# Performance work log

Hardware: AMD Instinct MI355X
Metric: run time of the kernel (lower is better)

Reference implementation:

```python
import jax, jax.numpy as jnp
import numpy as np

B, N, D, H = 4096, 64, 32, 64

def setup_inputs() -> dict:
    key = jax.random.key(0)
    ks = jax.random.split(key, 10)
    s = lambda fan_in: 1.0 / np.sqrt(fan_in)
    return {
        "joint_features": jax.random.normal(ks[0], (B, N, D), jnp.float32),
        "Wm1": jax.random.uniform(ks[1], (2 * D, H), jnp.float32, -s(2 * D), s(2 * D)),
        "bm1": jax.random.uniform(ks[2], (H,), jnp.float32, -s(2 * D), s(2 * D)),
        "Wm2": jax.random.uniform(ks[3], (H, D), jnp.float32, -s(H), s(H)),
        "bm2": jax.random.uniform(ks[4], (D,), jnp.float32, -s(H), s(H)),
        "Wu1": jax.random.uniform(ks[5], (2 * D, H), jnp.float32, -s(2 * D), s(2 * D)),
        "bu1": jax.random.uniform(ks[6], (H,), jnp.float32, -s(2 * D), s(2 * D)),
        "Wu2": jax.random.uniform(ks[7], (H, D), jnp.float32, -s(H), s(H)),
        "bu2": jax.random.uniform(ks[8], (D,), jnp.float32, -s(H), s(H)),
        "residual_weight": jnp.float32(0.5),
        "num_joints": N,
    }

def reference(joint_features, Wm1, bm1, Wm2, bm2, Wu1, bu1, Wu2, bu2, residual_weight, num_joints):
    n = num_joints
    # chain topology: directed edges (i->i+1) and (i+1->i); dst receives message
    dst = jnp.concatenate([jnp.arange(n - 1), jnp.arange(1, n)])  # [E]
    src = jnp.concatenate([jnp.arange(1, n), jnp.arange(n - 1)])  # [E]
    # edge gather + concat: [B, E, 2D]
    edge_in = jnp.concatenate([joint_features[:, dst], joint_features[:, src]], axis=-1)
    # message MLP (ReLU after both layers, per original Sequential)
    msg = jax.nn.relu(jax.nn.relu(edge_in @ Wm1 + bm1) @ Wm2 + bm2)  # [B, E, D]
    # scatter-add messages to destination nodes
    messages = jnp.zeros_like(joint_features).at[:, dst].add(msg)  # [B, N, D]
    # per-node update MLP on concat(feature, message)
    upd_in = jnp.concatenate([joint_features, messages], axis=-1)  # [B, N, 2D]
    updated = jax.nn.relu(upd_in @ Wu1 + bu1) @ Wu2 + bu2  # [B, N, D]
    return residual_weight * updated + (1.0 - residual_weight) * joint_features
```

## Files before the change

kernel.cpp:

```cpp
#include <hip/hip_runtime.h>
#include <hip/hip_bf16.h>


typedef __bf16 bf16x8 __attribute__((ext_vector_type(8)));
typedef float  f32x4  __attribute__((ext_vector_type(4)));
typedef unsigned short u16;

#define NBATCH 8
#define ITERS (NBATCH / 2)
#define HS 72
#define MS 40

#define FB2_OFF 0
#define FB3_OFF (FB2_OFF + 4 * 512)
#define FB4_OFF (FB3_OFF + 8 * 512)
#define SH_OFF   0
#define SM_OFF   (SH_OFF + 256 * HS)
#define BIAS_OFF (SM_OFF + 128 * MS)
#define SMEM_U16 (BIAS_OFF + 384)

__device__ __forceinline__ u16 f2b(float f) { return __builtin_bit_cast(u16, (__bf16)f); }
__device__ __forceinline__ f32x4 MFMA(bf16x8 a, bf16x8 b, f32x4 c) {
    return __builtin_amdgcn_mfma_f32_16x16x32_bf16(a, b, c, 0, 0, 0);
}
__device__ __forceinline__ bf16x8 pack8(float4 a, float4 b) {
    bf16x8 r = {(__bf16)a.x, (__bf16)a.y, (__bf16)a.z, (__bf16)a.w,
                (__bf16)b.x, (__bf16)b.y, (__bf16)b.z, (__bf16)b.w};
    return r;
}
__device__ __forceinline__ uint2 relu_pack4(f32x4 acc, f32x4 bias) {
    uint2 o;
    o.x = (unsigned)f2b(fmaxf(acc[0] + bias[0], 0.f)) |
          ((unsigned)f2b(fmaxf(acc[1] + bias[1], 0.f)) << 16);
    o.y = (unsigned)f2b(fmaxf(acc[2] + bias[2], 0.f)) |
          ((unsigned)f2b(fmaxf(acc[3] + bias[3], 0.f)) << 16);
    return o;
}
__device__ __forceinline__ void wave_lds_fence() {
    asm volatile("s_waitcnt lgkmcnt(0)" ::: "memory");
}
__device__ __forceinline__ void barrier_lds() {
    asm volatile("s_waitcnt lgkmcnt(0)" ::: "memory");
    __builtin_amdgcn_s_barrier();
    asm volatile("" ::: "memory");
}

__global__ __launch_bounds__(256, 2)
void agn_mfma(const float* __restrict__ x, const float* __restrict__ Wm1,
              const float* __restrict__ bm1, const float* __restrict__ Wm2,
              const float* __restrict__ bm2, const float* __restrict__ Wu1,
              const float* __restrict__ bu1, const float* __restrict__ Wu2,
              const float* __restrict__ bu2, const float* __restrict__ rw_p,
              float* __restrict__ out)
{
    __shared__ __align__(16) u16 smem[SMEM_U16];

    const int t = threadIdx.x;
    const int w = t >> 6;
    const int lane = t & 63;
    const int ln = lane & 15;
    const int q  = lane >> 4;
    const int bl = w >> 1;
    const int g0 = (w & 1) * 32;

    float* biasL = (float*)&smem[BIAS_OFF];

    if (t < 64)  { biasL[t] = bm1[t]; biasL[64 + t] = bu1[t]; }
    if (t < 32)  { biasL[128 + t] = bm2[t]; biasL[160 + t] = bu2[t]; }
    if (w == 0) {
#pragma unroll
        for (int ks = 0; ks < 2; ++ks)
#pragma unroll
            for (int s = 0; s < 2; ++s) {
                bf16x8 v;
#pragma unroll
                for (int j = 0; j < 8; ++j)
                    v[j] = (__bf16)Wm2[(ks * 32 + q * 8 + j) * 32 + s * 16 + ln];
                *(uint4*)&smem[FB2_OFF + (ks * 2 + s) * 512 + lane * 8] =
                    __builtin_bit_cast(uint4, v);
            }
    } else if (w == 1 || w == 2) {
        const int ks = w - 1;
#pragma unroll
        for (int ht = 0; ht < 4; ++ht) {
            bf16x8 v;
#pragma unroll
            for (int j = 0; j < 8; ++j)
                v[j] = (__bf16)Wu1[(ks * 32 + q * 8 + j) * 64 + ht * 16 + ln];
            *(uint4*)&smem[FB3_OFF + (ks * 4 + ht) * 512 + lane * 8] =
                __builtin_bit_cast(uint4, v);
        }
    } else {
#pragma unroll
        for (int ks = 0; ks < 2; ++ks)
#pragma unroll
            for (int s = 0; s < 2; ++s) {
                bf16x8 v;
#pragma unroll
                for (int j = 0; j < 8; ++j)
                    v[j] = (__bf16)Wu2[(ks * 32 + q * 8 + j) * 32 + s * 16 + ln];
                *(uint4*)&smem[FB4_OFF + (ks * 2 + s) * 512 + lane * 8] =
                    __builtin_bit_cast(uint4, v);
            }
    }

    bf16x8 B1a[4], B1b[4];
#pragma unroll
    for (int nt = 0; nt < 4; ++nt)
#pragma unroll
        for (int j = 0; j < 8; ++j) {
            B1a[nt][j] = (__bf16)Wm1[(q * 8 + j) * 64 + nt * 16 + ln];
            B1b[nt][j] = (__bf16)Wm1[(32 + q * 8 + j) * 64 + nt * 16 + ln];
        }

    barrier_lds();

    bf16x8 W2[2][2], W3[2][4], W4[2][2];
#pragma unroll
    for (int ks = 0; ks < 2; ++ks) {
#pragma unroll
        for (int s = 0; s < 2; ++s) {
            W2[ks][s] = __builtin_bit_cast(bf16x8, *(const uint4*)&smem[FB2_OFF + (ks * 2 + s) * 512 + lane * 8]);
            W4[ks][s] = __builtin_bit_cast(bf16x8, *(const uint4*)&smem[FB4_OFF + (ks * 2 + s) * 512 + lane * 8]);
        }
#pragma unroll
        for (int ht = 0; ht < 4; ++ht)
            W3[ks][ht] = __builtin_bit_cast(bf16x8, *(const uint4*)&smem[FB3_OFF + (ks * 4 + ht) * 512 + lane * 8]);
    }
    barrier_lds();

    const float rw = rw_p[0];
    const float om = 1.f - rw;
    const size_t base = (size_t)blockIdx.x * (NBATCH * 64 * 32);

    for (int it = 0; it < ITERS; ++it) {
        const float* xb = x + base + (size_t)(it * 2 + bl) * (64 * 32);
        float*       ob = out + base + (size_t)(it * 2 + bl) * (64 * 32);

        bf16x8 Xd[2];

#pragma unroll
        for (int nt = 0; nt < 2; ++nt) {
            const int n = g0 + nt * 16 + ln;
            const float* pd = xb + n * 32 + q * 8;
            float4 d0 = *(const float4*)pd, d1 = *(const float4*)(pd + 4);
            Xd[nt] = pack8(d0, d1);
            const int nn = (n == 63) ? n : n + 1;
            const int np = (n == 0)  ? n : n - 1;
            const float* pn = xb + nn * 32 + q * 8;
            const float* pp = xb + np * 32 + q * 8;
            float4 a0 = *(const float4*)pn, a1 = *(const float4*)(pn + 4);
            float4 b0 = *(const float4*)pp, b1 = *(const float4*)(pp + 4);
            bf16x8 Xn = pack8(a0, a1);
            bf16x8 Xp = pack8(b0, b1);
            u16* rf = &smem[SH_OFF + (w * 64 + nt * 16 + ln) * HS];
            u16* rb = &smem[SH_OFF + (w * 64 + 32 + nt * 16 + ln) * HS];
#pragma unroll
            for (int ht = 0; ht < 4; ++ht) {
                f32x4 bias = *(const f32x4*)&biasL[ht * 16 + q * 4];
                f32x4 af = {0.f, 0.f, 0.f, 0.f};
                af = MFMA(B1a[ht], Xd[nt], af);
                af = MFMA(B1b[ht], Xn, af);
                *(uint2*)&rf[ht * 16 + q * 4] = relu_pack4(af, bias);
                f32x4 ab = {0.f, 0.f, 0.f, 0.f};
                ab = MFMA(B1a[ht], Xd[nt], ab);
                ab = MFMA(B1b[ht], Xp, ab);
                *(uint2*)&rb[ht * 16 + q * 4] = relu_pack4(ab, bias);
            }
        }
        wave_lds_fence();

#pragma unroll
        for (int nt = 0; nt < 2; ++nt) {
            const int n = g0 + nt * 16 + ln;
            const u16* rf = &smem[SH_OFF + (w * 64 + nt * 16 + ln) * HS];
            const u16* rb = &smem[SH_OFF + (w * 64 + 32 + nt * 16 + ln) * HS];
            bf16x8 hf0 = __builtin_bit_cast(bf16x8, *(const uint4*)&rf[q * 8]);
            bf16x8 hf1 = __builtin_bit_cast(bf16x8, *(const uint4*)&rf[32 + q * 8]);
            bf16x8 hb0 = __builtin_bit_cast(bf16x8, *(const uint4*)&rb[q * 8]);
            bf16x8 hb1 = __builtin_bit_cast(bf16x8, *(const uint4*)&rb[32 + q * 8]);
#pragma unroll
            for (int s = 0; s < 2; ++s) {
                f32x4 bias = *(const f32x4*)&biasL[128 + s * 16 + q * 4];
                f32x4 cf = {0.f, 0.f, 0.f, 0.f};
                f32x4 cb = {0.f, 0.f, 0.f, 0.f};
                cf = MFMA(W2[0][s], hf0, cf); cf = MFMA(W2[1][s], hf1, cf);
                cb = MFMA(W2[0][s], hb0, cb); cb = MFMA(W2[1][s], hb1, cb);
                float m4[4];
#pragma unroll
                for (int r = 0; r < 4; ++r) {
                    float vf = (n != 63) ? fmaxf(cf[r] + bias[r], 0.f) : 0.f;
                    float vb = (n != 0)  ? fmaxf(cb[r] + bias[r], 0.f) : 0.f;
                    m4[r] = vf + vb;
                }
                uint2 o;
                o.x = (unsigned)f2b(m4[0]) | ((unsigned)f2b(m4[1]) << 16);
                o.y = (unsigned)f2b(m4[2]) | ((unsigned)f2b(m4[3]) << 16);
                *(uint2*)&smem[SM_OFF + (bl * 64 + n) * MS + s * 16 + q * 4] = o;
            }
        }
        wave_lds_fence();

#pragma unroll
        for (int nt = 0; nt < 2; ++nt) {
            const int n = g0 + nt * 16 + ln;
            bf16x8 A1 = __builtin_bit_cast(bf16x8, *(const uint4*)&smem[SM_OFF + (bl * 64 + n) * MS + q * 8]);
            u16* rh = &smem[SH_OFF + (w * 64 + nt * 16 + ln) * HS];
#pragma unroll
            for (int ht = 0; ht < 4; ++ht) {
                f32x4 bias = *(const f32x4*)&biasL[64 + ht * 16 + q * 4];
                f32x4 acc = {0.f, 0.f, 0.f, 0.f};
                acc = MFMA(W3[0][ht], Xd[nt], acc);
                acc = MFMA(W3[1][ht], A1, acc);
                *(uint2*)&rh[ht * 16 + q * 4] = relu_pack4(acc, bias);
            }
        }
        wave_lds_fence();

#pragma unroll
        for (int nt = 0; nt < 2; ++nt) {
            const int n = g0 + nt * 16 + ln;
            const u16* rh = &smem[SH_OFF + (w * 64 + nt * 16 + ln) * HS];
            bf16x8 A0 = __builtin_bit_cast(bf16x8, *(const uint4*)&rh[q * 8]);
            bf16x8 A1 = __builtin_bit_cast(bf16x8, *(const uint4*)&rh[32 + q * 8]);
#pragma unroll
            for (int s = 0; s < 2; ++s) {
                f32x4 bias = *(const f32x4*)&biasL[160 + s * 16 + q * 4];
                f32x4 acc = {0.f, 0.f, 0.f, 0.f};
                acc = MFMA(W4[0][s], A0, acc);
                acc = MFMA(W4[1][s], A1, acc);
                float4 xv = *(const float4*)(xb + n * 32 + s * 16 + q * 4);
                float4 o;
                o.x = rw * (acc[0] + bias[0]) + om * xv.x;
                o.y = rw * (acc[1] + bias[1]) + om * xv.y;
                o.z = rw * (acc[2] + bias[2]) + om * xv.z;
                o.w = rw * (acc[3] + bias[3]) + om * xv.w;
                *(float4*)(ob + n * 32 + s * 16 + q * 4) = o;
            }
        }
        wave_lds_fence();
    }
}

extern "C" void kernel_launch(void* const* d_in, const int* in_sizes, int n_in,
                              void* d_out, int out_size, void* d_ws, size_t ws_size,
                              hipStream_t stream) {
    const float* x   = (const float*)d_in[0];
    const float* Wm1 = (const float*)d_in[1];
    const float* bm1 = (const float*)d_in[2];
    const float* Wm2 = (const float*)d_in[3];
    const float* bm2 = (const float*)d_in[4];
    const float* Wu1 = (const float*)d_in[5];
    const float* bu1 = (const float*)d_in[6];
    const float* Wu2 = (const float*)d_in[7];
    const float* bu2 = (const float*)d_in[8];
    const float* rw  = (const float*)d_in[9];
    float* out = (float*)d_out;

    const int B = in_sizes[0] / (64 * 32);
    agn_mfma<<<B / NBATCH, 256, 0, stream>>>(x, Wm1, bm1, Wm2, bm2, Wu1, bu1, Wu2, bu2, rw, out);
}
```

Before: 120.2 us.

## Stage neighbor rows in LDS, prefetch next batch, fold biases into MFMA accumulators

Each wave now loads its 34-row window of joint features once per batch as bf16 into a private LDS tile and reads the centre, next and previous rows from LDS. Before, it issued three redundant global float4 loads per row. The next batch's window is prefetched into registers during the current batch's compute, and the residual x values are loaded early. Biases are used as the initial MFMA accumulator, and the shared Xd·B1a product is computed once for both edge directions, cutting MFMA count and VALU adds. This costs more LDS per block and extra registers for the prefetch buffers, which may reduce occupancy.

```diff
diff --git a/kernel.cpp b/kernel.cpp
--- a/kernel.cpp
+++ b/kernel.cpp
@@ -10,13 +10,15 @@
 #define ITERS (NBATCH / 2)
 #define HS 72
 #define MS 40
-
-#define FB2_OFF 0
-#define FB3_OFF (FB2_OFF + 4 * 512)
-#define FB4_OFF (FB3_OFF + 8 * 512)
-#define SH_OFF   0
-#define SM_OFF   (SH_OFF + 256 * HS)
-#define BIAS_OFF (SM_OFF + 128 * MS)
+#define XS 40
+
+#define SHW(w)  ((w) * (64 * HS))
+#define SMW(w)  (4 * 64 * HS + (w) * (32 * MS))
+#define SXW(w)  (23552 + (w) * (34 * XS))
+#define FB2_OFF  28992
+#define FB3_OFF  (FB2_OFF + 4 * 512)
+#define FB4_OFF  (FB3_OFF + 8 * 512)
+#define BIAS_OFF (FB4_OFF + 4 * 512)
 #define SMEM_U16 (BIAS_OFF + 384)
 
 __device__ __forceinline__ u16 f2b(float f) { return __builtin_bit_cast(u16, (__bf16)f); }
@@ -28,12 +30,10 @@
                 (__bf16)b.x, (__bf16)b.y, (__bf16)b.z, (__bf16)b.w};
     return r;
 }
-__device__ __forceinline__ uint2 relu_pack4(f32x4 acc, f32x4 bias) {
+__device__ __forceinline__ uint2 relu_pack4_nb(f32x4 acc) {
     uint2 o;
-    o.x = (unsigned)f2b(fmaxf(acc[0] + bias[0], 0.f)) |
-          ((unsigned)f2b(fmaxf(acc[1] + bias[1], 0.f)) << 16);
-    o.y = (unsigned)f2b(fmaxf(acc[2] + bias[2], 0.f)) |
-          ((unsigned)f2b(fmaxf(acc[3] + bias[3], 0.f)) << 16);
+    o.x = (unsigned)f2b(fmaxf(acc[0], 0.f)) | ((unsigned)f2b(fmaxf(acc[1], 0.f)) << 16);
+    o.y = (unsigned)f2b(fmaxf(acc[2], 0.f)) | ((unsigned)f2b(fmaxf(acc[3], 0.f)) << 16);
     return o;
 }
 __device__ __forceinline__ void wave_lds_fence() {
@@ -60,8 +60,8 @@
     const int lane = t & 63;
     const int ln = lane & 15;
     const int q  = lane >> 4;
-    const int bl = w >> 1;
     const int g0 = (w & 1) * 32;
+    const int shw = SHW(w), smw = SMW(w), sxw = SXW(w);
 
     float* biasL = (float*)&smem[BIAS_OFF];
 
@@ -133,108 +133,132 @@
     const float om = 1.f - rw;
     const size_t base = (size_t)blockIdx.x * (NBATCH * 64 * 32);
 
+    int goff[3], loff[3];
+#pragma unroll
+    for (int rnd = 0; rnd < 3; ++rnd) {
+        const int k = lane + 64 * rnd;
+        const int r = (k >> 2), ch = (k & 3);
+        int gn = g0 - 1 + r;
+        gn = gn < 0 ? 0 : (gn > 63 ? 63 : gn);
+        goff[rnd] = gn * 32 + ch * 8;
+        loff[rnd] = sxw + r * XS + ch * 8;
+    }
+
+    float4 pa[3], pb[3];
+    {
+        const float* xb0 = x + base + (size_t)(w >> 1) * (64 * 32);
+        pa[0] = *(const float4*)(xb0 + goff[0]); pb[0] = *(const float4*)(xb0 + goff[0] + 4);
+        pa[1] = *(const float4*)(xb0 + goff[1]); pb[1] = *(const float4*)(xb0 + goff[1] + 4);
+        if (lane < 8) { pa[2] = *(const float4*)(xb0 + goff[2]); pb[2] = *(const float4*)(xb0 + goff[2] + 4); }
+    }
+
     for (int it = 0; it < ITERS; ++it) {
-        const float* xb = x + base + (size_t)(it * 2 + bl) * (64 * 32);
-        float*       ob = out + base + (size_t)(it * 2 + bl) * (64 * 32);
+        const float* xb = x + base + (size_t)(it * 2 + (w >> 1)) * (64 * 32);
+        float*       ob = out + base + (size_t)(it * 2 + (w >> 1)) * (64 * 32);
+
+        *(uint4*)&smem[loff[0]] = __builtin_bit_cast(uint4, pack8(pa[0], pb[0]));
+        *(uint4*)&smem[loff[1]] = __builtin_bit_cast(uint4, pack8(pa[1], pb[1]));
+        if (lane < 8)
+            *(uint4*)&smem[loff[2]] = __builtin_bit_cast(uint4, pack8(pa[2], pb[2]));
+        wave_lds_fence();
+
+        if (it + 1 < ITERS) {
+            const float* xn = xb + 2 * (64 * 32);
+            pa[0] = *(const float4*)(xn + goff[0]); pb[0] = *(const float4*)(xn + goff[0] + 4);
+            pa[1] = *(const float4*)(xn + goff[1]); pb[1] = *(const float4*)(xn + goff[1] + 4);
+            if (lane < 8) { pa[2] = *(const float4*)(xn + goff[2]); pb[2] = *(const float4*)(xn + goff[2] + 4); }
+        }
 
         bf16x8 Xd[2];
 
 #pragma unroll
         for (int nt = 0; nt < 2; ++nt) {
-            const int n = g0 + nt * 16 + ln;
-            const float* pd = xb + n * 32 + q * 8;
-            float4 d0 = *(const float4*)pd, d1 = *(const float4*)(pd + 4);
-            Xd[nt] = pack8(d0, d1);
-            const int nn = (n == 63) ? n : n + 1;
-            const int np = (n == 0)  ? n : n - 1;
-            const float* pn = xb + nn * 32 + q * 8;
-            const float* pp = xb + np * 32 + q * 8;
-            float4 a0 = *(const float4*)pn, a1 = *(const float4*)(pn + 4);
-            float4 b0 = *(const float4*)pp, b1 = *(const float4*)(pp + 4);
-            bf16x8 Xn = pack8(a0, a1);
-            bf16x8 Xp = pack8(b0, b1);
-            u16* rf = &smem[SH_OFF + (w * 64 + nt * 16 + ln) * HS];
-            u16* rb = &smem[SH_OFF + (w * 64 + 32 + nt * 16 + ln) * HS];
+            const int nl = nt * 16 + ln;
+            const int r = nl + 1;
+            Xd[nt]    = __builtin_bit_cast(bf16x8, *(const uint4*)&smem[sxw + r * XS + q * 8]);
+            bf16x8 Xn = __builtin_bit_cast(bf16x8, *(const uint4*)&smem[sxw + (r + 1) * XS + q * 8]);
+            bf16x8 Xp = __builtin_bit_cast(bf16x8, *(const uint4*)&smem[sxw + (r - 1) * XS + q * 8]);
+            u16* rf = &smem[shw + nl * HS];
+            u16* rb = &smem[shw + (32 + nl) * HS];
 #pragma unroll
             for (int ht = 0; ht < 4; ++ht) {
-                f32x4 bias = *(const f32x4*)&biasL[ht * 16 + q * 4];
-                f32x4 af = {0.f, 0.f, 0.f, 0.f};
-                af = MFMA(B1a[ht], Xd[nt], af);
-                af = MFMA(B1b[ht], Xn, af);
-                *(uint2*)&rf[ht * 16 + q * 4] = relu_pack4(af, bias);
-                f32x4 ab = {0.f, 0.f, 0.f, 0.f};
-                ab = MFMA(B1a[ht], Xd[nt], ab);
-                ab = MFMA(B1b[ht], Xp, ab);
-                *(uint2*)&rb[ht * 16 + q * 4] = relu_pack4(ab, bias);
-            }
-        }
-        wave_lds_fence();
-
-#pragma unroll
-        for (int nt = 0; nt < 2; ++nt) {
-            const int n = g0 + nt * 16 + ln;
-            const u16* rf = &smem[SH_OFF + (w * 64 + nt * 16 + ln) * HS];
-            const u16* rb = &smem[SH_OFF + (w * 64 + 32 + nt * 16 + ln) * HS];
-            bf16x8 hf0 = __builtin_bit_cast(bf16x8, *(const uint4*)&rf[q * 8]);
-            bf16x8 hf1 = __builtin_bit_cast(bf16x8, *(const uint4*)&rf[32 + q * 8]);
-            bf16x8 hb0 = __builtin_bit_cast(bf16x8, *(const uint4*)&rb[q * 8]);
-            bf16x8 hb1 = __builtin_bit_cast(bf16x8, *(const uint4*)&rb[32 + q * 8]);
-#pragma unroll
-            for (int s = 0; s < 2; ++s) {
-                f32x4 bias = *(const f32x4*)&biasL[128 + s * 16 + q * 4];
-                f32x4 cf = {0.f, 0.f, 0.f, 0.f};
-                f32x4 cb = {0.f, 0.f, 0.f, 0.f};
-                cf = MFMA(W2[0][s], hf0, cf); cf = MFMA(W2[1][s], hf1, cf);
-                cb = MFMA(W2[0][s], hb0, cb); cb = MFMA(W2[1][s], hb1, cb);
+                f32x4 tt = *(const f32x4*)&biasL[ht * 16 + q * 4];
+                tt = MFMA(B1a[ht], Xd[nt], tt);
+                f32x4 af = MFMA(B1b[ht], Xn, tt);
+                f32x4 ab = MFMA(B1b[ht], Xp, tt);
+                *(uint2*)&rf[ht * 16 + q * 4] = relu_pack4_nb(af);
+                *(uint2*)&rb[ht * 16 + q * 4] = relu_pack4_nb(ab);
+            }
+        }
+        wave_lds_fence();
+
+#pragma unroll
+        for (int nt = 0; nt < 2; ++nt) {
+            const int nl = nt * 16 + ln;
+            const int n = g0 + nl;
+            bf16x8 hf0 = __builtin_bit_cast(bf16x8, *(const uint4*)&smem[shw + nl * HS + q * 8]);
+            bf16x8 hf1 = __builtin_bit_cast(bf16x8, *(const uint4*)&smem[shw + nl * HS + 32 + q * 8]);
+            bf16x8 hb0 = __builtin_bit_cast(bf16x8, *(const uint4*)&smem[shw + (32 + nl) * HS + q * 8]);
+            bf16x8 hb1 = __builtin_bit_cast(bf16x8, *(const uint4*)&smem[shw + (32 + nl) * HS + 32 + q * 8]);
+#pragma unroll
+            for (int s = 0; s < 2; ++s) {
+                f32x4 bb = *(const f32x4*)&biasL[128 + s * 16 + q * 4];
+                f32x4 cf = MFMA(W2[0][s], hf0, bb); cf = MFMA(W2[1][s], hf1, cf);
+                f32x4 cb = MFMA(W2[0][s], hb0, bb); cb = MFMA(W2[1][s], hb1, cb);
                 float m4[4];
 #pragma unroll
                 for (int r = 0; r < 4; ++r) {
-                    float vf = (n != 63) ? fmaxf(cf[r] + bias[r], 0.f) : 0.f;
-                    float vb = (n != 0)  ? fmaxf(cb[r] + bias[r], 0.f) : 0.f;
+                    float vf = (n != 63) ? fmaxf(cf[r], 0.f) : 0.f;
+                    float vb = (n != 0)  ? fmaxf(cb[r], 0.f) : 0.f;
                     m4[r] = vf + vb;
                 }
                 uint2 o;
                 o.x = (unsigned)f2b(m4[0]) | ((unsigned)f2b(m4[1]) << 16);
                 o.y = (unsigned)f2b(m4[2]) | ((unsigned)f2b(m4[3]) << 16);
-                *(uint2*)&smem[SM_OFF + (bl * 64 + n) * MS + s * 16 + q * 4] = o;
-            }
-        }
-        wave_lds_fence();
-
-#pragma unroll
-        for (int nt = 0; nt < 2; ++nt) {
-            const int n = g0 + nt * 16 + ln;
-            bf16x8 A1 = __builtin_bit_cast(bf16x8, *(const uint4*)&smem[SM_OFF + (bl * 64 + n) * MS + q * 8]);
-            u16* rh = &smem[SH_OFF + (w * 64 + nt * 16 + ln) * HS];
+                *(uint2*)&smem[smw + nl * MS + s * 16 + q * 4] = o;
+            }
+        }
+
+        float4 xvp[2][2];
+#pragma unroll
+        for (int nt = 0; nt < 2; ++nt)
+#pragma unroll
+            for (int s = 0; s < 2; ++s)
+                xvp[nt][s] = *(const float4*)(xb + (g0 + nt * 16 + ln) * 32 + s * 16 + q * 4);
+
+        wave_lds_fence();
+
+#pragma unroll
+        for (int nt = 0; nt < 2; ++nt) {
+            const int nl = nt * 16 + ln;
+            bf16x8 A1 = __builtin_bit_cast(bf16x8, *(const uint4*)&smem[smw + nl * MS + q * 8]);
 #pragma unroll
             for (int ht = 0; ht < 4; ++ht) {
-                f32x4 bias = *(const f32x4*)&biasL[64 + ht * 16 + q * 4];
-                f32x4 acc = {0.f, 0.f, 0.f, 0.f};
-                acc = MFMA(W3[0][ht], Xd[nt], acc);
-                acc = MFMA(W3[1][ht], A1, acc);
-                *(uint2*)&rh[ht * 16 + q * 4] = relu_pack4(acc, bias);
-            }
-        }
-        wave_lds_fence();
-
-#pragma unroll
-        for (int nt = 0; nt < 2; ++nt) {
-            const int n = g0 + nt * 16 + ln;
-            const u16* rh = &smem[SH_OFF + (w * 64 + nt * 16 + ln) * HS];
-            bf16x8 A0 = __builtin_bit_cast(bf16x8, *(const uint4*)&rh[q * 8]);
-            bf16x8 A1 = __builtin_bit_cast(bf16x8, *(const uint4*)&rh[32 + q * 8]);
-#pragma unroll
-            for (int s = 0; s < 2; ++s) {
-                f32x4 bias = *(const f32x4*)&biasL[160 + s * 16 + q * 4];
-                f32x4 acc = {0.f, 0.f, 0.f, 0.f};
-                acc = MFMA(W4[0][s], A0, acc);
-                acc = MFMA(W4[1][s], A1, acc);
-                float4 xv = *(const float4*)(xb + n * 32 + s * 16 + q * 4);
+                f32x4 tt = *(const f32x4*)&biasL[64 + ht * 16 + q * 4];
+                tt = MFMA(W3[0][ht], Xd[nt], tt);
+                tt = MFMA(W3[1][ht], A1, tt);
+                *(uint2*)&smem[shw + nl * HS + ht * 16 + q * 4] = relu_pack4_nb(tt);
+            }
+        }
+        wave_lds_fence();
+
+#pragma unroll
+        for (int nt = 0; nt < 2; ++nt) {
+            const int nl = nt * 16 + ln;
+            const int n = g0 + nl;
+            bf16x8 A0 = __builtin_bit_cast(bf16x8, *(const uint4*)&smem[shw + nl * HS + q * 8]);
+            bf16x8 A1 = __builtin_bit_cast(bf16x8, *(const uint4*)&smem[shw + nl * HS + 32 + q * 8]);
+#pragma unroll
+            for (int s = 0; s < 2; ++s) {
+                f32x4 tt = *(const f32x4*)&biasL[160 + s * 16 + q * 4];
+                tt = MFMA(W4[0][s], A0, tt);
+                tt = MFMA(W4[1][s], A1, tt);
+                const float4 xv = xvp[nt][s];
                 float4 o;
-                o.x = rw * (acc[0] + bias[0]) + om * xv.x;
-                o.y = rw * (acc[1] + bias[1]) + om * xv.y;
-                o.z = rw * (acc[2] + bias[2]) + om * xv.z;
-                o.w = rw * (acc[3] + bias[3]) + om * xv.w;
+                o.x = rw * tt[0] + om * xv.x;
+                o.y = rw * tt[1] + om * xv.y;
+                o.z = rw * tt[2] + om * xv.z;
+                o.w = rw * tt[3] + om * xv.w;
                 *(float4*)(ob + n * 32 + s * 16 + q * 4) = o;
             }
         }
```

After: 108.5 us. 1.11x faster.
